# Performance work log

Hardware: AMD Instinct MI355X
Metric: run time of the kernel (lower is better)

## Reference

```python
import jax, jax.numpy as jnp
import numpy as np
import math

N_HEADS = 32
N_KV_HEADS = 8
HEAD_DIM = 64
THETA = 10000.0
NEG_INF = -1e9


def _rope_cos_sin(seq_len, dim, dtype=jnp.float32):
    # freqs over even indices, matching torch.arange(0, dim, 2)/dim
    freqs = 1.0 / (THETA ** (jnp.arange(0, dim, 2, dtype=jnp.float32) / dim))  # [dim/2]
    angles = jnp.arange(seq_len, dtype=jnp.float32)[:, None] * freqs[None, :]  # [S, dim/2]
    return jnp.cos(angles).astype(dtype), jnp.sin(angles).astype(dtype)


def _apply_rope(x, cos, sin):
    # x: [B, S, H, D]; pairs (x[...,2i], x[...,2i+1]) rotated as complex numbers
    xr = x[..., 0::2]
    xi = x[..., 1::2]
    # broadcast cos/sin [S, D/2] -> [1, S, 1, D/2]
    c = cos[None, :, None, :]
    s = sin[None, :, None, :]
    or_ = xr * c - xi * s
    oi_ = xr * s + xi * c
    # interleave back: [..., D/2, 2] -> [..., D]
    return jnp.stack([or_, oi_], axis=-1).reshape(x.shape)


def setup_inputs() -> dict:
    key = jax.random.key(0)
    ks = jax.random.split(key, 5)
    B, S, D = 2, 2048, 2048
    KV_D = N_KV_HEADS * HEAD_DIM
    x = jax.random.normal(ks[0], (B, S, D), dtype=jnp.float32)
    sc = 1.0 / math.sqrt(D)
    wq = jax.random.normal(ks[1], (D, D), dtype=jnp.float32) * sc
    wk = jax.random.normal(ks[2], (D, KV_D), dtype=jnp.float32) * sc
    wv = jax.random.normal(ks[3], (D, KV_D), dtype=jnp.float32) * sc
    wo = jax.random.normal(ks[4], (D, D), dtype=jnp.float32) * sc
    # additive causal mask [1, 1, S, S]
    causal = jnp.tril(jnp.ones((S, S), dtype=bool))
    mask = jnp.where(causal, 0.0, NEG_INF).astype(jnp.float32)[None, None]
    return {"x": x, "mask": mask, "wq": wq, "wk": wk, "wv": wv, "wo": wo}


def reference(x, mask, wq, wk, wv, wo):
    B, S, D = x.shape
    n_rep = N_HEADS // N_KV_HEADS
    q = (x @ wq).reshape(B, S, N_HEADS, HEAD_DIM)
    k = (x @ wk).reshape(B, S, N_KV_HEADS, HEAD_DIM)
    v = (x @ wv).reshape(B, S, N_KV_HEADS, HEAD_DIM)
    cos, sin = _rope_cos_sin(S, HEAD_DIM)
    q = _apply_rope(q, cos, sin)
    k = _apply_rope(k, cos, sin)
    # GQA: repeat_interleave kv heads along head dim
    k = jnp.repeat(k, n_rep, axis=2)  # [B, S, H, D]
    v = jnp.repeat(v, n_rep, axis=2)
    scores = jnp.einsum("bqhd,bkhd->bhqk", q, k) / math.sqrt(HEAD_DIM)
    scores = scores + mask
    probs = jax.nn.softmax(scores.astype(jnp.float32), axis=-1).astype(q.dtype)
    out = jnp.einsum("bhqk,bkhd->bqhd", probs, v).reshape(B, S, N_HEADS * HEAD_DIM)
    return out @ wo
```

## Files before the change

### kernel.cpp

```cpp
#include <hip/hip_runtime.h>
#include <hip/hip_bf16.h>


#define S_LEN 2048
#define BATCH 2
#define D_MODEL 2048
#define NH 32
#define NKV 8
#define HD 64
#define KV_D (NKV * HD)
#define QKV_N (D_MODEL + 2 * KV_D)

typedef __attribute__((ext_vector_type(8))) short short8;
typedef __attribute__((ext_vector_type(4))) float float4v;
typedef __attribute__((ext_vector_type(16))) float f32x16;
typedef __attribute__((ext_vector_type(2))) unsigned uint2v;

typedef __attribute__((address_space(1))) const unsigned int gu32;
typedef __attribute__((address_space(3))) unsigned int lu32;

#if __has_builtin(__builtin_amdgcn_exp2f)
#define PEXP(x) __builtin_amdgcn_exp2f(x)
#else
#define PEXP(x) __expf((x) * 0.69314718f)
#endif
#define QSCALE 0.18033688f

__device__ __forceinline__ float bf2f(unsigned short u) {
    unsigned x = ((unsigned)u) << 16;
    return __builtin_bit_cast(float, x);
}
__device__ __forceinline__ unsigned short f2bf(float f) {
    unsigned u = __builtin_bit_cast(unsigned, f);
    unsigned r = (u + 0x7fffu + ((u >> 16) & 1u)) >> 16;
    return (unsigned short)r;
}

__device__ __forceinline__ unsigned cvt_pk_bf16(float a, float b) {
    unsigned r;
    asm("v_cvt_pk_bf16_f32 %0, %1, %2" : "=v"(r) : "v"(a), "v"(b));
    return r;
}

__device__ __forceinline__ void pl32swap(unsigned a, unsigned b,
                                         unsigned& x, unsigned& y) {
#if __has_builtin(__builtin_amdgcn_permlane32_swap)
    uint2v r = __builtin_amdgcn_permlane32_swap(a, b, false, false);
    x = r[0];
    y = r[1];
#else
    unsigned pa = (unsigned)__shfl_xor((int)a, 32);
    unsigned pb = (unsigned)__shfl_xor((int)b, 32);
    bool lo = (threadIdx.x & 63) < 32;
    x = lo ? a : pb;
    y = lo ? pa : b;
#endif
}

__global__ void cast_f32_bf16(const float* __restrict__ in,
                              unsigned short* __restrict__ out, long n) {
    long i = ((long)blockIdx.x * 256 + threadIdx.x) * 4;
    if (i + 3 >= n) return;
    const float4v v = *(const float4v*)&in[i];
    unsigned short o[4];
    o[0] = f2bf(v[0]); o[1] = f2bf(v[1]); o[2] = f2bf(v[2]); o[3] = f2bf(v[3]);
    *(__attribute__((ext_vector_type(4))) short*)&out[i] =
        *(__attribute__((ext_vector_type(4))) short*)o;
}

__global__ __launch_bounds__(256) void wtrans(const float* __restrict__ in,
                                              unsigned short* __restrict__ out,
                                              int K, int N) {
    __shared__ unsigned short t[32 * 33];
    const int nb = blockIdx.x * 32, kb = blockIdx.y * 32;
    const int c = threadIdx.x & 31, rr = threadIdx.x >> 5;
#pragma unroll
    for (int it = 0; it < 4; ++it) {
        int r = it * 8 + rr;
        t[c * 33 + r] = f2bf(in[(long)(kb + r) * N + nb + c]);
    }
    __syncthreads();
#pragma unroll
    for (int it = 0; it < 4; ++it) {
        int r = it * 8 + rr;
        out[(long)(nb + r) * K + kb + c] = t[r * 33 + c];
    }
}

template <int TM, bool F32OUT>
__global__ __launch_bounds__(256, TM == 64 ? 4 : 3)
void gemm_sw(const unsigned short* __restrict__ A,
             const unsigned short* __restrict__ BT,
             void* __restrict__ Cv, int M, int N, int K) {
    __shared__ unsigned short As[TM * 64];
    __shared__ unsigned short Bs[128 * 64];
    const int tid = threadIdx.x;
    const int wid = tid >> 6, lane = tid & 63;
    const int l15 = lane & 15, quad = lane >> 4;
    const int wm = (wid >> 1) * (TM / 2), wn = (wid & 1) * 64;
    const int row0 = blockIdx.x * TM, col0 = blockIdx.y * 128;
    constexpr int MI = TM / 32;

    float4v acc[MI][4];
    float4v z;
    z[0] = z[1] = z[2] = z[3] = 0.0f;
    for (int mi = 0; mi < MI; ++mi)
        for (int ni = 0; ni < 4; ++ni) acc[mi][ni] = z;

    const int r_ld = lane >> 3;
    const int swz_ld = ((lane & 7) ^ (lane >> 3)) * 8;
    const int sw = l15 & 7;

    for (int kb = 0; kb < K; kb += 64) {
        __syncthreads();
#pragma unroll
        for (int c = 0; c < 4; ++c) {
            int chunk = c * 4 + wid;
            int r = chunk * 8 + r_ld;
            __builtin_amdgcn_global_load_lds(
                (gu32*)&BT[(long)(col0 + r) * K + kb + swz_ld],
                (lu32*)&Bs[chunk * 512], 16, 0, 0);
            if (c < MI)
                __builtin_amdgcn_global_load_lds(
                    (gu32*)&A[(long)(row0 + r) * K + kb + swz_ld],
                    (lu32*)&As[chunk * 512], 16, 0, 0);
        }
        __syncthreads();
#pragma unroll
        for (int kk = 0; kk < 64; kk += 32) {
            short8 af[MI], bf[4];
#pragma unroll
            for (int i = 0; i < MI; ++i)
                af[i] = *(const short8*)
                    &As[(wm + i * 16 + l15) * 64 + ((((kk >> 3) + quad) ^ sw) << 3)];
#pragma unroll
            for (int i = 0; i < 4; ++i)
                bf[i] = *(const short8*)
                    &Bs[(wn + i * 16 + l15) * 64 + ((((kk >> 3) + quad) ^ sw) << 3)];
#pragma unroll
            for (int mi = 0; mi < MI; ++mi)
#pragma unroll
                for (int ni = 0; ni < 4; ++ni)
                    acc[mi][ni] = __builtin_amdgcn_mfma_f32_16x16x32_bf16(
                        af[mi], bf[ni], acc[mi][ni], 0, 0, 0);
        }
    }
#pragma unroll
    for (int mi = 0; mi < MI; ++mi)
#pragma unroll
        for (int ni = 0; ni < 4; ++ni)
#pragma unroll
            for (int r = 0; r < 4; ++r) {
                int m = row0 + wm + mi * 16 + quad * 4 + r;
                int n = col0 + wn + ni * 16 + l15;
                if (F32OUT)
                    ((float*)Cv)[(long)m * N + n] = acc[mi][ni][r];
                else
                    ((unsigned short*)Cv)[(long)m * N + n] = f2bf(acc[mi][ni][r]);
            }
}

__global__ __launch_bounds__(256) void rope2(unsigned short* __restrict__ qkv) {
    const int i = threadIdx.x & 31;
    const int row = blockIdx.x * 8 + (threadIdx.x >> 5);
    const int s = row & (S_LEN - 1);
    float freq = __expf(-0.28782313f * (float)i);
    float ang = (float)s * freq;
    float c = cosf(ang), sn = sinf(ang);
    unsigned* p = (unsigned*)qkv + ((long)row * QKV_N + 2 * i) / 2;
#pragma unroll
    for (int head = 0; head < 40; ++head) {
        const float qs = (head < 32) ? QSCALE : 1.0f;
        unsigned v = p[head * 32];
        float xr = bf2f((unsigned short)(v & 0xffff));
        float xi = bf2f((unsigned short)(v >> 16));
        unsigned short lo = f2bf((xr * c - xi * sn) * qs);
        unsigned short hi = f2bf((xr * sn + xi * c) * qs);
        p[head * 32] = (unsigned)lo | ((unsigned)hi << 16);
    }
}

__global__ __launch_bounds__(256) void vtrans(const unsigned short* __restrict__ qkv,
                                              unsigned short* __restrict__ Vt) {
    __shared__ unsigned t[64 * 33];
    const int st = blockIdx.x * 64, kh = blockIdx.y, b = blockIdx.z;
    const int tid = threadIdx.x;
    {
        const int r2 = tid >> 3, dbase = (tid & 7) * 8;
        const unsigned short* src =
            qkv + ((long)(b * S_LEN + st + 2 * r2)) * QKV_N + D_MODEL + KV_D + kh * HD + dbase;
        short8 lo = *(const short8*)src;
        short8 hi = *(const short8*)(src + QKV_N);
#pragma unroll
        for (int j = 0; j < 8; ++j)
            t[(dbase + j) * 33 + r2] =
                (unsigned)(unsigned short)lo[j] | ((unsigned)(unsigned short)hi[j] << 16);
    }
    __syncthreads();
    {
        const int d = tid >> 2, sb = (tid & 3) * 8;
        unsigned short o[16];
#pragma unroll
        for (int jj = 0; jj < 8; ++jj) {
            unsigned v = t[d * 33 + sb + jj];
            o[2 * jj] = (unsigned short)(v & 0xffff);
            o[2 * jj + 1] = (unsigned short)(v >> 16);
        }
        unsigned short* dst =
            Vt + ((long)((b * 8 + kh) * 64 + d)) * S_LEN + st + sb * 2;
        *(short8*)dst = *(short8*)&o[0];
        *(short8*)(dst + 8) = *(short8*)&o[8];
    }
}

__global__ __launch_bounds__(512, 4) void flash8(const unsigned short* __restrict__ qkv,
                                                 const unsigned short* __restrict__ Vt,
                                                 unsigned short* __restrict__ O) {
    __shared__ unsigned short Ks[4][64 * 64];
    __shared__ unsigned short Vs[4][64 * 64];

    const int tid = threadIdx.x, w = tid >> 6, lane = tid & 63;
    const int g = w & 3, p = w >> 2;
    const int l31 = lane & 31, hi = lane >> 5;
    const int r7 = l31 & 7;
    const int h = blockIdx.y, b = blockIdx.z;
    const int kh = h >> 2, bkh = b * 8 + kh;
    const int qtA = blockIdx.x;

    const int sr = lane >> 3;
    const int sc = ((lane & 7) ^ sr) * 8;
    const unsigned short* Kg =
        qkv + (long)b * S_LEN * QKV_N + D_MODEL + kh * HD + sc;
    const unsigned short* Vg = Vt + ((long)bkh * 64) * S_LEN + sc;

#define STAGE8(pb)                                                                   \
    do {                                                                             \
        const int tt = (pb) + p;                                                     \
        const int bt = tt & 3;                                                       \
        const long kk0 = (long)tt * 64;                                              \
        __builtin_amdgcn_global_load_lds(                                            \
            (gu32*)&Kg[(kk0 + g * 16 + sr) * QKV_N],                                 \
            (lu32*)&Ks[bt][(g * 16) * 64], 16, 0, 0);                                \
        __builtin_amdgcn_global_load_lds(                                            \
            (gu32*)&Kg[(kk0 + g * 16 + 8 + sr) * QKV_N],                             \
            (lu32*)&Ks[bt][(g * 16 + 8) * 64], 16, 0, 0);                            \
        __builtin_amdgcn_global_load_lds(                                            \
            (gu32*)&Vg[(long)(g * 16 + sr) * S_LEN + kk0],                           \
            (lu32*)&Vs[bt][(g * 16) * 64], 16, 0, 0);                                \
        __builtin_amdgcn_global_load_lds(                                            \
            (gu32*)&Vg[(long)(g * 16 + 8 + sr) * S_LEN + kk0],                       \
            (lu32*)&Vs[bt][(g * 16 + 8) * 64], 16, 0, 0);                            \
    } while (0)

    for (int tsel = 0; tsel < 2; ++tsel) {
        const int qt = tsel ? (15 - qtA) : qtA;
        const int row_w = qt * 128 + g * 32;
        const int nkt = 2 * qt + 2;
        const int nss = nkt >> 1;

        short8 aq[4];
        {
            const long qbase = ((long)(b * S_LEN) + row_w + l31) * QKV_N + h * HD + hi * 8;
#pragma unroll
            for (int ks = 0; ks < 4; ++ks) aq[ks] = *(const short8*)&qkv[qbase + ks * 16];
        }

        f32x16 oacc[2] = {};
        float lp = 0.0f;

        STAGE8(0);
        __syncthreads();

        for (int ss = 0; ss < nss; ++ss) {
            const int t = 2 * ss + p;
            const int k0 = t * 64;
            const int bt = t & 3;
            if (2 * ss + 2 < nkt) STAGE8(2 * ss + 2);

            if (row_w + 31 >= k0) {
                const bool mb = (k0 + 63 > row_w);
#pragma unroll
                for (int kb2 = 0; kb2 < 2; ++kb2) {
                    short8 kf[4];
#pragma unroll
                    for (int ks = 0; ks < 4; ++ks)
                        kf[ks] = *(const short8*)
                            &Ks[bt][(kb2 * 32 + l31) * 64 + (((ks * 2 + hi) ^ r7) << 3)];
                    f32x16 s = {};
                    __builtin_amdgcn_s_setprio(1);
#pragma unroll
                    for (int ks = 0; ks < 4; ++ks)
                        s = __builtin_amdgcn_mfma_f32_32x32x16_bf16(kf[ks], aq[ks], s, 0, 0, 0);
                    __builtin_amdgcn_s_setprio(0);

                    const int qrel = row_w + l31 - k0 - kb2 * 32 - 4 * hi;
#pragma unroll
                    for (int r = 0; r < 16; ++r) {
                        float v = s[r];
                        if (mb && ((r & 3) + 8 * (r >> 2) > qrel)) v = -1e4f;
                        float pv = PEXP(v);
                        lp += pv;
                        s[r] = pv;
                    }

#pragma unroll
                    for (int ksl = 0; ksl < 2; ++ksl) {
                        const int gx = ksl * 8;
                        unsigned ca = cvt_pk_bf16(s[gx + 0], s[gx + 1]);
                        unsigned cb = cvt_pk_bf16(s[gx + 2], s[gx + 3]);
                        unsigned cc = cvt_pk_bf16(s[gx + 4], s[gx + 5]);
                        unsigned cd = cvt_pk_bf16(s[gx + 6], s[gx + 7]);
                        unsigned dw0, dw1, dw2, dw3;
                        pl32swap(ca, cc, dw0, dw2);
                        pl32swap(cb, cd, dw1, dw3);
                        union { unsigned u[4]; short8 v8; } pf;
                        pf.u[0] = dw0; pf.u[1] = dw1; pf.u[2] = dw2; pf.u[3] = dw3;
                        const int lc = kb2 * 4 + ksl * 2 + hi;
                        __builtin_amdgcn_s_setprio(1);
#pragma unroll
                        for (int dblk = 0; dblk < 2; ++dblk) {
                            short8 vf = *(const short8*)
                                &Vs[bt][(dblk * 32 + l31) * 64 + ((lc ^ r7) << 3)];
                            oacc[dblk] = __builtin_amdgcn_mfma_f32_32x32x16_bf16(
                                vf, pf.v8, oacc[dblk], 0, 0, 0);
                        }
                        __builtin_amdgcn_s_setprio(0);
                    }
                }
            }
            __syncthreads();
        }

        float* mV = (float*)&Vs[0][0];
        float* mL = (float*)&Ks[2][0];
        if (p == 1) {
#pragma unroll
            for (int dblk = 0; dblk < 2; ++dblk)
#pragma unroll
                for (int r = 0; r < 16; ++r)
                    mV[(g * 32 + dblk * 16 + r) * 64 + lane] = oacc[dblk][r];
            mL[g * 64 + lane] = lp;
        }
        __syncthreads();
        if (p == 0) {
#pragma unroll
            for (int dblk = 0; dblk < 2; ++dblk)
#pragma unroll
                for (int r = 0; r < 16; ++r)
                    oacc[dblk][r] += mV[(g * 32 + dblk * 16 + r) * 64 + lane];
            lp += mL[g * 64 + lane];

            float linv = 1.0f / (lp + __shfl_xor(lp, 32));
            unsigned short* Oe = &Ks[0][0] + g * 2048;
#pragma unroll
            for (int dblk = 0; dblk < 2; ++dblk)
#pragma unroll
                for (int rq = 0; rq < 4; ++rq) {
                    unsigned plo = cvt_pk_bf16(oacc[dblk][rq * 4 + 0] * linv,
                                               oacc[dblk][rq * 4 + 1] * linv);
                    unsigned phi = cvt_pk_bf16(oacc[dblk][rq * 4 + 2] * linv,
                                               oacc[dblk][rq * 4 + 3] * linv);
                    uint2v wv;
                    wv[0] = plo; wv[1] = phi;
                    int e = l31 * 64 + (((rq + 4 * dblk) ^ r7) << 3) + hi * 4;
                    *(uint2v*)&Oe[e] = wv;
                }
#pragma unroll
            for (int i = 0; i < 4; ++i) {
                int q2 = i * 8 + (lane >> 3);
                int e = q2 * 64 + (((lane & 7) ^ (lane >> 3)) << 3);
                short8 ov = *(const short8*)&Oe[e];
                long orow = ((long)(b * S_LEN) + row_w + q2) * D_MODEL + h * HD + (lane & 7) * 8;
                *(short8*)&O[orow] = ov;
            }
        }
        __syncthreads();
    }
#undef STAGE8
}

extern "C" void kernel_launch(void* const* d_in, const int* in_sizes, int n_in,
                              void* d_out, int out_size, void* d_ws, size_t ws_size,
                              hipStream_t stream) {
    const float* x  = (const float*)d_in[0];
    const float* wq = (const float*)d_in[n_in - 4];
    const float* wk = (const float*)d_in[n_in - 3];
    const float* wv = (const float*)d_in[n_in - 2];
    const float* wo = (const float*)d_in[n_in - 1];
    float* out = (float*)d_out;

    unsigned short* ws    = (unsigned short*)d_ws;
    unsigned short* xb    = ws;
    unsigned short* Obuf  = ws;
    unsigned short* qkv   = xb + (long)BATCH * S_LEN * D_MODEL;
    unsigned short* woT   = qkv + (long)BATCH * S_LEN * QKV_N;
    unsigned short* wqkvT = woT + (long)D_MODEL * D_MODEL;
    unsigned short* Vt    = wqkvT;

    const int M = BATCH * S_LEN;
    const long xn = (long)M * D_MODEL;

    cast_f32_bf16<<<(int)(xn / 4 / 256), 256, 0, stream>>>(x, xb, xn);

    wtrans<<<dim3(D_MODEL / 32, D_MODEL / 32), 256, 0, stream>>>(wq, wqkvT, D_MODEL, D_MODEL);
    wtrans<<<dim3(KV_D / 32, D_MODEL / 32), 256, 0, stream>>>(wk, wqkvT + (long)D_MODEL * D_MODEL, D_MODEL, KV_D);
    wtrans<<<dim3(KV_D / 32, D_MODEL / 32), 256, 0, stream>>>(wv, wqkvT + (long)(D_MODEL + KV_D) * D_MODEL, D_MODEL, KV_D);
    wtrans<<<dim3(D_MODEL / 32, D_MODEL / 32), 256, 0, stream>>>(wo, woT, D_MODEL, D_MODEL);

    gemm_sw<128, false><<<dim3(M / 128, QKV_N / 128), 256, 0, stream>>>(
        xb, wqkvT, qkv, M, QKV_N, D_MODEL);

    rope2<<<M / 8, 256, 0, stream>>>(qkv);

    vtrans<<<dim3(S_LEN / 64, NKV, BATCH), 256, 0, stream>>>(qkv, Vt);

    flash8<<<dim3(8, NH, BATCH), 512, 0, stream>>>(qkv, Vt, Obuf);

    gemm_sw<64, true><<<dim3(M / 64, D_MODEL / 128), 256, 0, stream>>>(
        Obuf, woT, out, M, D_MODEL, D_MODEL);
}
```

Baseline: 310.7 us.

## Merge prep kernels, fuse Q RoPE into attention, combine K-RoPE with V transpose

Folds the five input cast/transpose kernels into one launch and merges K RoPE with the V transpose, which removes launch gaps. Q RoPE and the softmax scale now happen inside the attention kernel as Q fragments load, so the separate pass no longer reads and writes the Q columns. The output projection GEMM switches from 64-row to 128-row tiles. The cost is extra transcendental math per Q load in the attention prologue and half as many blocks for the output GEMM.

```diff
diff --git a/kernel.cpp b/kernel.cpp
--- a/kernel.cpp
+++ b/kernel.cpp
@@ -57,22 +57,46 @@
 #endif
 }
 
-__global__ void cast_f32_bf16(const float* __restrict__ in,
-                              unsigned short* __restrict__ out, long n) {
-    long i = ((long)blockIdx.x * 256 + threadIdx.x) * 4;
-    if (i + 3 >= n) return;
-    const float4v v = *(const float4v*)&in[i];
-    unsigned short o[4];
-    o[0] = f2bf(v[0]); o[1] = f2bf(v[1]); o[2] = f2bf(v[2]); o[3] = f2bf(v[3]);
-    *(__attribute__((ext_vector_type(4))) short*)&out[i] =
-        *(__attribute__((ext_vector_type(4))) short*)o;
-}
-
-__global__ __launch_bounds__(256) void wtrans(const float* __restrict__ in,
-                                              unsigned short* __restrict__ out,
-                                              int K, int N) {
+__global__ __launch_bounds__(256) void prep(const float* __restrict__ x,
+                                            const float* __restrict__ wq,
+                                            const float* __restrict__ wk,
+                                            const float* __restrict__ wv,
+                                            const float* __restrict__ wo,
+                                            unsigned short* __restrict__ xb,
+                                            unsigned short* __restrict__ wqkvT,
+                                            unsigned short* __restrict__ woT) {
     __shared__ unsigned short t[32 * 33];
-    const int nb = blockIdx.x * 32, kb = blockIdx.y * 32;
+    const int bx = blockIdx.x;
+    if (bx >= 10240) {
+        long i = ((long)(bx - 10240) * 256 + threadIdx.x) * 4;
+        const long n = (long)BATCH * S_LEN * D_MODEL;
+        if (i + 3 >= n) return;
+        const float4v v = *(const float4v*)&x[i];
+        unsigned short o[4];
+        o[0] = f2bf(v[0]); o[1] = f2bf(v[1]); o[2] = f2bf(v[2]); o[3] = f2bf(v[3]);
+        *(__attribute__((ext_vector_type(4))) short*)&xb[i] =
+            *(__attribute__((ext_vector_type(4))) short*)o;
+        return;
+    }
+    const float* in;
+    unsigned short* out;
+    int N, nb, kb;
+    if (bx < 4096) {
+        in = wq; out = wqkvT; N = 2048;
+        nb = (bx & 63) * 32; kb = (bx >> 6) * 32;
+    } else if (bx < 5120) {
+        const int i2 = bx - 4096;
+        in = wk; out = wqkvT + (long)D_MODEL * D_MODEL; N = 512;
+        nb = (i2 & 15) * 32; kb = (i2 >> 4) * 32;
+    } else if (bx < 6144) {
+        const int i2 = bx - 5120;
+        in = wv; out = wqkvT + (long)(D_MODEL + KV_D) * D_MODEL; N = 512;
+        nb = (i2 & 15) * 32; kb = (i2 >> 4) * 32;
+    } else {
+        const int i2 = bx - 6144;
+        in = wo; out = woT; N = 2048;
+        nb = (i2 & 63) * 32; kb = (i2 >> 6) * 32;
+    }
     const int c = threadIdx.x & 31, rr = threadIdx.x >> 5;
 #pragma unroll
     for (int it = 0; it < 4; ++it) {
@@ -83,7 +107,7 @@
 #pragma unroll
     for (int it = 0; it < 4; ++it) {
         int r = it * 8 + rr;
-        out[(long)(nb + r) * K + kb + c] = t[r * 33 + c];
+        out[(long)(nb + r) * D_MODEL + kb + c] = t[r * 33 + c];
     }
 }
 
@@ -160,31 +184,31 @@
             }
 }
 
-__global__ __launch_bounds__(256) void rope2(unsigned short* __restrict__ qkv) {
-    const int i = threadIdx.x & 31;
-    const int row = blockIdx.x * 8 + (threadIdx.x >> 5);
-    const int s = row & (S_LEN - 1);
-    float freq = __expf(-0.28782313f * (float)i);
-    float ang = (float)s * freq;
-    float c = cosf(ang), sn = sinf(ang);
-    unsigned* p = (unsigned*)qkv + ((long)row * QKV_N + 2 * i) / 2;
-#pragma unroll
-    for (int head = 0; head < 40; ++head) {
-        const float qs = (head < 32) ? QSCALE : 1.0f;
-        unsigned v = p[head * 32];
-        float xr = bf2f((unsigned short)(v & 0xffff));
-        float xi = bf2f((unsigned short)(v >> 16));
-        unsigned short lo = f2bf((xr * c - xi * sn) * qs);
-        unsigned short hi = f2bf((xr * sn + xi * c) * qs);
-        p[head * 32] = (unsigned)lo | ((unsigned)hi << 16);
-    }
-}
-
-__global__ __launch_bounds__(256) void vtrans(const unsigned short* __restrict__ qkv,
-                                              unsigned short* __restrict__ Vt) {
+__global__ __launch_bounds__(256) void ropek_vtrans(unsigned short* __restrict__ qkv,
+                                                    unsigned short* __restrict__ Vt) {
     __shared__ unsigned t[64 * 33];
-    const int st = blockIdx.x * 64, kh = blockIdx.y, b = blockIdx.z;
-    const int tid = threadIdx.x;
+    const int bx = blockIdx.x, tid = threadIdx.x;
+    if (bx < 512) {
+        const int i = tid & 31;
+        const int row = bx * 8 + (tid >> 5);
+        const int s = row & (S_LEN - 1);
+        float freq = __expf(-0.28782313f * (float)i);
+        float ang = (float)s * freq;
+        float c = cosf(ang), sn = sinf(ang);
+        unsigned* p = (unsigned*)qkv + ((long)row * QKV_N + 2 * i) / 2;
+#pragma unroll
+        for (int head = 32; head < 40; ++head) {
+            unsigned v = p[head * 32];
+            float xr = bf2f((unsigned short)(v & 0xffff));
+            float xi = bf2f((unsigned short)(v >> 16));
+            unsigned short lo = f2bf(xr * c - xi * sn);
+            unsigned short hi = f2bf(xr * sn + xi * c);
+            p[head * 32] = (unsigned)lo | ((unsigned)hi << 16);
+        }
+        return;
+    }
+    const int idx = bx - 512;
+    const int st = (idx & 31) * 64, kh = (idx >> 5) & 7, b = idx >> 8;
     {
         const int r2 = tid >> 3, dbase = (tid & 7) * 8;
         const unsigned short* src =
@@ -213,7 +237,7 @@
     }
 }
 
-__global__ __launch_bounds__(512, 4) void flash8(const unsigned short* __restrict__ qkv,
+__global__ __launch_bounds__(512, 4) void flash9(const unsigned short* __restrict__ qkv,
                                                  const unsigned short* __restrict__ Vt,
                                                  unsigned short* __restrict__ O) {
     __shared__ unsigned short Ks[4][64 * 64];
@@ -233,7 +257,7 @@
         qkv + (long)b * S_LEN * QKV_N + D_MODEL + kh * HD + sc;
     const unsigned short* Vg = Vt + ((long)bkh * 64) * S_LEN + sc;
 
-#define STAGE8(pb)                                                                   \
+#define STAGE9(pb)                                                                   \
     do {                                                                             \
         const int tt = (pb) + p;                                                     \
         const int bt = tt & 3;                                                       \
@@ -261,21 +285,36 @@
         short8 aq[4];
         {
             const long qbase = ((long)(b * S_LEN) + row_w + l31) * QKV_N + h * HD + hi * 8;
-#pragma unroll
-            for (int ks = 0; ks < 4; ++ks) aq[ks] = *(const short8*)&qkv[qbase + ks * 16];
+            const float fs = (float)(row_w + l31);
+#pragma unroll
+            for (int ks = 0; ks < 4; ++ks) {
+                short8 v = *(const short8*)&qkv[qbase + ks * 16];
+                short8 o;
+#pragma unroll
+                for (int jp = 0; jp < 4; ++jp) {
+                    const int ii = ks * 8 + hi * 4 + jp;
+                    float ang = fs * __expf(-0.28782313f * (float)ii);
+                    float c = cosf(ang), sn = sinf(ang);
+                    float xr = bf2f((unsigned short)v[2 * jp]);
+                    float xi = bf2f((unsigned short)v[2 * jp + 1]);
+                    o[2 * jp] = (short)f2bf((xr * c - xi * sn) * QSCALE);
+                    o[2 * jp + 1] = (short)f2bf((xr * sn + xi * c) * QSCALE);
+                }
+                aq[ks] = o;
+            }
         }
 
         f32x16 oacc[2] = {};
         float lp = 0.0f;
 
-        STAGE8(0);
+        STAGE9(0);
         __syncthreads();
 
         for (int ss = 0; ss < nss; ++ss) {
             const int t = 2 * ss + p;
             const int k0 = t * 64;
             const int bt = t & 3;
-            if (2 * ss + 2 < nkt) STAGE8(2 * ss + 2);
+            if (2 * ss + 2 < nkt) STAGE9(2 * ss + 2);
 
             if (row_w + 31 >= k0) {
                 const bool mb = (k0 + 63 > row_w);
@@ -376,7 +415,7 @@
         }
         __syncthreads();
     }
-#undef STAGE8
+#undef STAGE9
 }
 
 extern "C" void kernel_launch(void* const* d_in, const int* in_sizes, int n_in,
@@ -398,24 +437,16 @@
     unsigned short* Vt    = wqkvT;
 
     const int M = BATCH * S_LEN;
-    const long xn = (long)M * D_MODEL;
-
-    cast_f32_bf16<<<(int)(xn / 4 / 256), 256, 0, stream>>>(x, xb, xn);
-
-    wtrans<<<dim3(D_MODEL / 32, D_MODEL / 32), 256, 0, stream>>>(wq, wqkvT, D_MODEL, D_MODEL);
-    wtrans<<<dim3(KV_D / 32, D_MODEL / 32), 256, 0, stream>>>(wk, wqkvT + (long)D_MODEL * D_MODEL, D_MODEL, KV_D);
-    wtrans<<<dim3(KV_D / 32, D_MODEL / 32), 256, 0, stream>>>(wv, wqkvT + (long)(D_MODEL + KV_D) * D_MODEL, D_MODEL, KV_D);
-    wtrans<<<dim3(D_MODEL / 32, D_MODEL / 32), 256, 0, stream>>>(wo, woT, D_MODEL, D_MODEL);
+
+    prep<<<18432, 256, 0, stream>>>(x, wq, wk, wv, wo, xb, wqkvT, woT);
 
     gemm_sw<128, false><<<dim3(M / 128, QKV_N / 128), 256, 0, stream>>>(
         xb, wqkvT, qkv, M, QKV_N, D_MODEL);
 
-    rope2<<<M / 8, 256, 0, stream>>>(qkv);
-
-    vtrans<<<dim3(S_LEN / 64, NKV, BATCH), 256, 0, stream>>>(qkv, Vt);
-
-    flash8<<<dim3(8, NH, BATCH), 512, 0, stream>>>(qkv, Vt, Obuf);
-
-    gemm_sw<64, true><<<dim3(M / 64, D_MODEL / 128), 256, 0, stream>>>(
+    ropek_vtrans<<<1024, 256, 0, stream>>>(qkv, Vt);
+
+    flash9<<<dim3(8, NH, BATCH), 512, 0, stream>>>(qkv, Vt, Obuf);
+
+    gemm_sw<128, true><<<dim3(M / 128, D_MODEL / 128), 256, 0, stream>>>(
         Obuf, woT, out, M, D_MODEL, D_MODEL);
 }
```

Result: slower. 328.9 us (+5.9%).
